# Optimization experiments

Measured on AMD Instinct MI355X. Metric: run time of the kernel, lower is better.

Reference implementation:

```python
import jax, jax.numpy as jnp
import numpy as np

N = 50000
E = 800000
NFEAT = 128
NHID = 64
NCLASS = 40


def setup_inputs() -> dict:
    key = jax.random.key(0)
    ks = jax.random.split(key, 12)
    return {
        "x": jax.random.normal(ks[0], (N, NFEAT), dtype=jnp.float32),
        "M": jax.random.uniform(ks[1], (N, 1), dtype=jnp.float32),
        "AM": jax.random.uniform(ks[2], (N, 1), dtype=jnp.float32),
        "adj_vals": jax.random.uniform(ks[3], (E,), dtype=jnp.float32),
        "adjZ_vals": jax.random.uniform(ks[4], (E,), dtype=jnp.float32),
        "W0": jax.random.normal(ks[5], (NFEAT, NFEAT), dtype=jnp.float32) * (1.414 / np.sqrt(NFEAT)),
        "b0": jnp.zeros((NFEAT,), dtype=jnp.float32),
        "W1": jax.random.normal(ks[6], (NFEAT, NHID), dtype=jnp.float32) * (1.414 / np.sqrt(NFEAT)),
        "b1": jnp.zeros((NHID,), dtype=jnp.float32),
        "W2": jax.random.normal(ks[7], (NHID, NCLASS), dtype=jnp.float32) * (1.0 / np.sqrt(NHID)),
        "b2": jnp.zeros((NCLASS,), dtype=jnp.float32),
        "row": jax.random.randint(ks[8], (E,), 0, N, dtype=jnp.int32),
        "col": jax.random.randint(ks[9], (E,), 0, N, dtype=jnp.int32),
    }


def _spmm(vals, row, col, X, n):
    # sparse (COO) @ dense: out[r] = sum_e vals[e] * X[col[e]] for row[e]==r
    return jax.ops.segment_sum(vals[:, None] * X[col], row, num_segments=n)


def reference(x, M, AM, adj_vals, adjZ_vals, W0, b0, W1, b1, W2, b2, row, col):
    n = x.shape[0]
    # gc0: PaGConv(nfeat->nfeat) on adjZ, then ReLU (dropout is identity in eval)
    h = _spmm(adjZ_vals, row, col, M * x, n) * AM
    h = jax.nn.relu(h @ W0 + b0)
    # gc1: PaGConv(nfeat->nhid) on adjZ, then ReLU
    h = _spmm(adjZ_vals, row, col, M * h, n) * AM
    h = jax.nn.relu(h @ W1 + b1)
    # gc2: plain GConv(nhid->nclass) on adj
    h = _spmm(adj_vals, row, col, h, n)
    h = h @ W2 + b2
    return jax.nn.log_softmax(h, axis=1)
```

## Files before the change

kernel.cpp:

```cpp
#include <hip/hip_runtime.h>
#include <hip/hip_bf16.h>
#include <math.h>


__device__ __forceinline__ float rl_f(float v, int j) {
    return __builtin_bit_cast(float,
        __builtin_amdgcn_readlane(__builtin_bit_cast(int, v), j));
}
__device__ __forceinline__ int rl_i(int v, int j) {
    return __builtin_amdgcn_readlane(v, j);
}
__device__ __forceinline__ unsigned short f2bf(float f) {
    unsigned u = __builtin_bit_cast(unsigned, f);
    u += 0x7fffu + ((u >> 16) & 1u);
    return (unsigned short)(u >> 16);
}
__device__ __forceinline__ float bf_lo(unsigned u) {
    return __builtin_bit_cast(float, u << 16);
}
__device__ __forceinline__ float bf_hi(unsigned u) {
    return __builtin_bit_cast(float, u & 0xffff0000u);
}


template <int K, int COLS, int CPT, bool MSCALE>
__device__ __forceinline__ void gemm_body(float* __restrict__ smem,
                                          const float* __restrict__ A,
                                          const float* __restrict__ Mv,
                                          const float* __restrict__ W,
                                          unsigned short* __restrict__ out, int n, int bid) {
    constexpr int TC = COLS / CPT;
    constexpr int RG = 256 / TC;
    constexpr int RPT = 8;
    constexpr int ROWS = RG * RPT;
    constexpr int KT = 32;
    constexpr int AP = KT + 4;
    static_assert(COLS % CPT == 0 && 256 % TC == 0, "bad tiling");

    float* As = smem;
    float* Ws = smem + ROWS * AP;

    const int t = threadIdx.x;
    const int rg = t / TC;
    const int c0 = (t % TC) * CPT;
    const int r0 = bid * ROWS;

    float acc[RPT][CPT];
#pragma unroll
    for (int i = 0; i < RPT; ++i)
#pragma unroll
        for (int c = 0; c < CPT; ++c) acc[i][c] = 0.0f;

    for (int k0 = 0; k0 < K; k0 += KT) {
        __syncthreads();
        for (int e = t; e < ROWS * (KT / 4); e += 256) {
            const int row = e / (KT / 4);
            const int kq = e % (KT / 4);
            const int r = r0 + row;
            float4 v = make_float4(0.f, 0.f, 0.f, 0.f);
            if (r < n) {
                v = *(const float4*)&A[(size_t)r * K + k0 + kq * 4];
                if constexpr (MSCALE) {
                    const float m = Mv[r];
                    v.x *= m; v.y *= m; v.z *= m; v.w *= m;
                }
            }
            *(float4*)&As[row * AP + kq * 4] = v;
        }
        for (int i = t * 4; i < KT * COLS; i += 1024)
            *(float4*)&Ws[i] = *(const float4*)&W[(size_t)k0 * COLS + i];
        __syncthreads();

#pragma unroll
        for (int kk = 0; kk < KT; kk += 4) {
            float w[4][CPT];
#pragma unroll
            for (int kj = 0; kj < 4; ++kj)
#pragma unroll
                for (int c = 0; c < CPT; ++c)
                    w[kj][c] = Ws[(kk + kj) * COLS + c0 + c];
#pragma unroll
            for (int i = 0; i < RPT; ++i) {
                const float4 av = *(const float4*)&As[(rg + i * RG) * AP + kk];
#pragma unroll
                for (int c = 0; c < CPT; ++c) {
                    acc[i][c] += av.x * w[0][c];
                    acc[i][c] += av.y * w[1][c];
                    acc[i][c] += av.z * w[2][c];
                    acc[i][c] += av.w * w[3][c];
                }
            }
        }
    }

#pragma unroll
    for (int i = 0; i < RPT; ++i) {
        const int r = r0 + rg + i * RG;
        if (r >= n) continue;
        if constexpr (CPT == 4) {
            ushort4 o;
            o.x = f2bf(acc[i][0]); o.y = f2bf(acc[i][1]);
            o.z = f2bf(acc[i][2]); o.w = f2bf(acc[i][3]);
            *(ushort4*)&out[(size_t)r * COLS + c0] = o;
        } else {
#pragma unroll
            for (int c = 0; c < CPT; ++c)
                out[(size_t)r * COLS + c0 + c] = f2bf(acc[i][c]);
        }
    }
}

template <int K, int COLS, int CPT, bool MSCALE>
__launch_bounds__(256)
__global__ void gemm_tile(const float* __restrict__ A, const float* __restrict__ Mv,
                          const float* __restrict__ W, unsigned short* __restrict__ out, int n) {
    constexpr int TC = COLS / CPT;
    constexpr int RG = 256 / TC;
    constexpr int ROWS = RG * 8;
    __shared__ float smem[ROWS * 36 + 32 * COLS];
    gemm_body<K, COLS, CPT, MSCALE>(smem, A, Mv, W, out, n, blockIdx.x);
}


__launch_bounds__(256)
__global__ void gemm0_hist(const float* __restrict__ x, const float* __restrict__ Mv,
                           const float* __restrict__ W0, unsigned short* __restrict__ t_buf,
                           const int* __restrict__ row, int* __restrict__ cnt,
                           int* __restrict__ pos_local, int n, int E, int gemmBlocks) {
    __shared__ float smem[64 * 36 + 32 * 128];
    const int b = blockIdx.x;
    if (b < gemmBlocks) {
        gemm_body<128, 128, 4, true>(smem, x, Mv, W0, t_buf, n, b);
    } else {
        const int e = (b - gemmBlocks) * 256 + threadIdx.x;
        if (e < E) pos_local[e] = atomicAdd(&cnt[row[e]], 1);
    }
}


__global__ void scan_part(const int* __restrict__ cnt, int* __restrict__ out,
                          int* __restrict__ bsums, int n) {
    __shared__ int sdata[256];
    const int t = threadIdx.x;
    const int base = blockIdx.x * 1024 + t * 4;
    int v[4];
#pragma unroll
    for (int i = 0; i < 4; ++i) v[i] = (base + i < n) ? cnt[base + i] : 0;
    int tsum = v[0] + v[1] + v[2] + v[3];
    sdata[t] = tsum;
    __syncthreads();
    for (int off = 1; off < 256; off <<= 1) {
        int x = (t >= off) ? sdata[t - off] : 0;
        __syncthreads();
        sdata[t] += x;
        __syncthreads();
    }
    int run = sdata[t] - tsum;
    if (t == 255) bsums[blockIdx.x] = sdata[t];
#pragma unroll
    for (int i = 0; i < 4; ++i) {
        if (base + i < n) out[base + i] = run;
        run += v[i];
    }
}

__global__ void scan_top(int* __restrict__ bs, int nb) {
    int t = threadIdx.x;
    int orig = (t < nb) ? bs[t] : 0;
    int v = orig;
#pragma unroll
    for (int off = 1; off < 64; off <<= 1) {
        int x = __shfl_up(v, off);
        if (t >= off) v += x;
    }
    if (t < nb) bs[t] = v - orig;
}

__global__ void scan_add(int* __restrict__ rp, const int* __restrict__ bs,
                         int n, int total) {
    int i = blockIdx.x * blockDim.x + threadIdx.x;
    if (i < n) rp[i] += bs[i >> 10];
    if (i == 0) rp[n] = total;
}


__global__ void scatter_kernel(const int* __restrict__ row, const int* __restrict__ col,
                               const float* __restrict__ vA, const float* __restrict__ vZ,
                               const int* __restrict__ rp, const int* __restrict__ pos_local,
                               float* __restrict__ packed, int E) {
    int e = blockIdx.x * blockDim.x + threadIdx.x;
    if (e >= E) return;
    const int pos = rp[row[e]] + pos_local[e];
    float3 pk;
    pk.x = __int_as_float(col[e]);
    pk.y = vZ[e];
    pk.z = vA[e];
    *(float3*)&packed[(size_t)3 * pos] = pk;
}


__launch_bounds__(256)
__global__ void spmm128_kernel(const float* __restrict__ packed,
                               const int* __restrict__ rp, const unsigned short* __restrict__ X,
                               const float* __restrict__ AM, const float* __restrict__ bias,
                               float* __restrict__ out, int n) {
    const int lane = threadIdx.x & 63;
    const int r = (int)((blockIdx.x * (unsigned)blockDim.x + threadIdx.x) >> 6);
    if (r >= n) return;
    const int s = __builtin_amdgcn_readfirstlane(rp[r]);
    const int e = __builtin_amdgcn_readfirstlane(rp[r + 1]);

    float acc0 = 0.0f, acc1 = 0.0f;
    for (int base = s; base < e; base += 64) {
        const int nn = min(64, e - base);
        int ci = 0; float vf = 0.0f;
        if (lane < nn) {
            const float3 pk = *(const float3*)&packed[(size_t)3 * (base + lane)];
            ci = __builtin_bit_cast(int, pk.x);
            vf = pk.y;
        }
        int j = 0;
        for (; j + 8 <= nn; j += 8) {
            unsigned u[8];
#pragma unroll
            for (int q = 0; q < 8; ++q) {
                const int cq = rl_i(ci, j + q);
                u[q] = *(const unsigned*)(X + (size_t)cq * 128 + lane * 2);
            }
#pragma unroll
            for (int q = 0; q < 8; ++q) {
                const float vq = rl_f(vf, j + q);
                acc0 += vq * bf_lo(u[q]);
                acc1 += vq * bf_hi(u[q]);
            }
        }
        for (; j < nn; ++j) {
            const int cq = rl_i(ci, j);
            const float vq = rl_f(vf, j);
            const unsigned u = *(const unsigned*)(X + (size_t)cq * 128 + lane * 2);
            acc0 += vq * bf_lo(u);
            acc1 += vq * bf_hi(u);
        }
    }

    const float am = AM[r];
    float o0 = acc0 * am + bias[2 * lane];
    float o1 = acc1 * am + bias[2 * lane + 1];
    o0 = fmaxf(o0, 0.0f); o1 = fmaxf(o1, 0.0f);
    *(float2*)(out + (size_t)r * 128 + lane * 2) = make_float2(o0, o1);
}


__launch_bounds__(256)
__global__ void spmm64_kernel(const float* __restrict__ packed,
                              const int* __restrict__ rp, const unsigned short* __restrict__ X,
                              const float* __restrict__ AM, const float* __restrict__ bias,
                              float* __restrict__ out, int n) {
    const int lane = threadIdx.x & 63;
    const int g = lane >> 5;
    const int ls = lane & 31;
    const int r = (int)((blockIdx.x * (unsigned)blockDim.x + threadIdx.x) >> 6);
    if (r >= n) return;
    const int s = __builtin_amdgcn_readfirstlane(rp[r]);
    const int e = __builtin_amdgcn_readfirstlane(rp[r + 1]);

    float acc0 = 0.0f, acc1 = 0.0f;
    for (int base = s; base < e; base += 64) {
        const int nn = min(64, e - base);
        int ci = 0; float vf = 0.0f;
        if (lane < nn) {
            const float3 pk = *(const float3*)&packed[(size_t)3 * (base + lane)];
            ci = __builtin_bit_cast(int, pk.x);
            vf = pk.y;
        }
        for (int j = 0; j < nn; j += 8) {
#pragma unroll
            for (int q = 0; q < 4; ++q) {
                const int jj = j + 2 * q + g;
                const bool ok = jj < nn;
                const int idx = jj & 63;
                const int c = __shfl(ci, idx);
                const float v = __shfl(vf, idx);
                if (ok) {
                    const unsigned u = *(const unsigned*)(X + (size_t)c * 64 + ls * 2);
                    acc0 += v * bf_lo(u);
                    acc1 += v * bf_hi(u);
                }
            }
        }
    }
    acc0 += __shfl_xor(acc0, 32);
    acc1 += __shfl_xor(acc1, 32);

    if (lane < 32) {
        const float am = AM[r];
        float o0 = acc0 * am + bias[2 * ls];
        float o1 = acc1 * am + bias[2 * ls + 1];
        o0 = fmaxf(o0, 0.0f); o1 = fmaxf(o1, 0.0f);
        *(float2*)(out + (size_t)r * 64 + ls * 2) = make_float2(o0, o1);
    }
}


__launch_bounds__(256)
__global__ void spmm40_kernel(const float* __restrict__ packed,
                              const int* __restrict__ rp, const unsigned short* __restrict__ X,
                              const float* __restrict__ bias,
                              float* __restrict__ out, int n) {
    const int lane = threadIdx.x & 63;
    const int g = lane / 20;
    const int ls = lane - 20 * g;
    const bool active = g < 3;
    const int r = (int)((blockIdx.x * (unsigned)blockDim.x + threadIdx.x) >> 6);
    if (r >= n) return;
    const int s = __builtin_amdgcn_readfirstlane(rp[r]);
    const int e = __builtin_amdgcn_readfirstlane(rp[r + 1]);

    float acc0 = 0.0f, acc1 = 0.0f;
    for (int base = s; base < e; base += 64) {
        const int nn = min(64, e - base);
        int ci = 0; float vf = 0.0f;
        if (lane < nn) {
            const float3 pk = *(const float3*)&packed[(size_t)3 * (base + lane)];
            ci = __builtin_bit_cast(int, pk.x);
            vf = pk.z;
        }
        for (int j = 0; j < nn; j += 12) {
#pragma unroll
            for (int q = 0; q < 4; ++q) {
                const int jj = j + 3 * q + g;
                const bool ok = active && jj < nn;
                const int idx = jj & 63;
                const int c = __shfl(ci, idx);
                const float v = __shfl(vf, idx);
                if (ok) {
                    const unsigned u = *(const unsigned*)(X + (size_t)c * 40 + ls * 2);
                    acc0 += v * bf_lo(u);
                    acc1 += v * bf_hi(u);
                }
            }
        }
    }
    {
        const float a1 = __shfl(acc0, (lane + 20) & 63);
        const float a2 = __shfl(acc0, (lane + 40) & 63);
        const float b1 = __shfl(acc1, (lane + 20) & 63);
        const float b2 = __shfl(acc1, (lane + 40) & 63);
        acc0 += a1 + a2;
        acc1 += b1 + b2;
    }

    const bool own = lane < 20;
    const float vv0 = own ? (acc0 + bias[2 * ls]) : -INFINITY;
    const float vv1 = own ? (acc1 + bias[2 * ls + 1]) : -INFINITY;
    float mx = fmaxf(vv0, vv1);
#pragma unroll
    for (int off = 32; off > 0; off >>= 1) mx = fmaxf(mx, __shfl_xor(mx, off));
    float sum = own ? (expf(vv0 - mx) + expf(vv1 - mx)) : 0.0f;
#pragma unroll
    for (int off = 32; off > 0; off >>= 1) sum += __shfl_xor(sum, off);
    if (own) {
        const float lse = mx + logf(sum);
        *(float2*)(out + (size_t)r * 40 + ls * 2) = make_float2(vv0 - lse, vv1 - lse);
    }
}


extern "C" void kernel_launch(void* const* d_in, const int* in_sizes, int n_in,
                              void* d_out, int out_size, void* d_ws, size_t ws_size,
                              hipStream_t stream) {
    const float* x    = (const float*)d_in[0];
    const float* M    = (const float*)d_in[1];
    const float* AM   = (const float*)d_in[2];
    const float* adjv = (const float*)d_in[3];
    const float* adjZ = (const float*)d_in[4];
    const float* W0   = (const float*)d_in[5];
    const float* b0   = (const float*)d_in[6];
    const float* W1   = (const float*)d_in[7];
    const float* b1   = (const float*)d_in[8];
    const float* W2   = (const float*)d_in[9];
    const float* b2   = (const float*)d_in[10];
    const int* row    = (const int*)d_in[11];
    const int* col    = (const int*)d_in[12];
    float* out = (float*)d_out;

    const int n = in_sizes[1];
    const int E = in_sizes[3];

    float* t_f   = (float*)d_ws;
    unsigned short* t_buf = (unsigned short*)t_f;
    float* h_buf = t_f + (size_t)n * 128;
    int* cnt     = (int*)(h_buf + (size_t)n * 128);
    int* rp      = cnt + n;
    int* bsums   = rp + (n + 1);
    float* packed = (float*)(bsums + 64);
    int* pos_local = (int*)h_buf;

    hipMemsetAsync(cnt, 0, (size_t)n * sizeof(int), stream);

    const int gemm0Blocks = (n + 63) / 64;
    const int histBlocks  = (E + 255) / 256;
    gemm0_hist<<<gemm0Blocks + histBlocks, 256, 0, stream>>>(x, M, W0, t_buf, row, cnt,
                                                             pos_local, n, E, gemm0Blocks);

    const int nblk = (n + 1023) >> 10;
    scan_part<<<nblk, 256, 0, stream>>>(cnt, rp, bsums, n);
    scan_top<<<1, 64, 0, stream>>>(bsums, nblk);
    scan_add<<<(n + 255) / 256, 256, 0, stream>>>(rp, bsums, n, E);
    scatter_kernel<<<(E + 255) / 256, 256, 0, stream>>>(row, col, adjv, adjZ, rp,
                                                        pos_local, packed, E);

    const int spmmBlocks = (n + 3) / 4;

    spmm128_kernel<<<spmmBlocks, 256, 0, stream>>>(packed, rp, t_buf, AM, b0, h_buf, n);
    gemm_tile<128, 64, 4, true><<<(n + 127) / 128, 256, 0, stream>>>(h_buf, M, W1, t_buf, n);
    spmm64_kernel<<<spmmBlocks, 256, 0, stream>>>(packed, rp, t_buf, AM, b1, h_buf, n);
    gemm_tile<64, 40, 5, false><<<(n + 255) / 256, 256, 0, stream>>>(h_buf, nullptr, W2, t_buf, n);
    spmm40_kernel<<<spmmBlocks, 256, 0, stream>>>(packed, rp, t_buf, b2, out, n);
}
```

Before: 289.8 us.

## Replace FP32 tiled GEMMs with bf16 MFMA GEMMs and bf16 intermediate activations

Replaces the shared-memory FP32 GEMM tiles with MFMA 16x16x32 bf16 matrix instructions, using weights pre-transposed and converted to bf16 by a new small prep kernel. The SpMM kernels now write their ReLU outputs as packed bf16 instead of fp32, and the M row-scaling is folded into spmm128's epilogue, which halves intermediate traffic and lets the GEMMs read bf16 directly. Values are clamped before bf16 conversion. The cost is an extra kernel launch and lower precision in the GEMM inputs.

```diff
diff --git a/kernel.cpp b/kernel.cpp
--- a/kernel.cpp
+++ b/kernel.cpp
@@ -2,6 +2,9 @@
 #include <hip/hip_bf16.h>
 #include <math.h>
 
+
+typedef __attribute__((ext_vector_type(8))) short bf16x8;
+typedef __attribute__((ext_vector_type(4))) float f32x4;
 
 __device__ __forceinline__ float rl_f(float v, int j) {
     return __builtin_bit_cast(float,
@@ -15,122 +18,124 @@
     u += 0x7fffu + ((u >> 16) & 1u);
     return (unsigned short)(u >> 16);
 }
+__device__ __forceinline__ unsigned pack2bf(float lo, float hi) {
+    return (unsigned)f2bf(lo) | ((unsigned)f2bf(hi) << 16);
+}
 __device__ __forceinline__ float bf_lo(unsigned u) {
     return __builtin_bit_cast(float, u << 16);
 }
 __device__ __forceinline__ float bf_hi(unsigned u) {
     return __builtin_bit_cast(float, u & 0xffff0000u);
 }
-
-
-template <int K, int COLS, int CPT, bool MSCALE>
-__device__ __forceinline__ void gemm_body(float* __restrict__ smem,
-                                          const float* __restrict__ A,
-                                          const float* __restrict__ Mv,
-                                          const float* __restrict__ W,
-                                          unsigned short* __restrict__ out, int n, int bid) {
-    constexpr int TC = COLS / CPT;
-    constexpr int RG = 256 / TC;
-    constexpr int RPT = 8;
-    constexpr int ROWS = RG * RPT;
-    constexpr int KT = 32;
-    constexpr int AP = KT + 4;
-    static_assert(COLS % CPT == 0 && 256 % TC == 0, "bad tiling");
-
-    float* As = smem;
-    float* Ws = smem + ROWS * AP;
-
-    const int t = threadIdx.x;
-    const int rg = t / TC;
-    const int c0 = (t % TC) * CPT;
-    const int r0 = bid * ROWS;
-
-    float acc[RPT][CPT];
-#pragma unroll
-    for (int i = 0; i < RPT; ++i)
-#pragma unroll
-        for (int c = 0; c < CPT; ++c) acc[i][c] = 0.0f;
-
-    for (int k0 = 0; k0 < K; k0 += KT) {
-        __syncthreads();
-        for (int e = t; e < ROWS * (KT / 4); e += 256) {
-            const int row = e / (KT / 4);
-            const int kq = e % (KT / 4);
-            const int r = r0 + row;
-            float4 v = make_float4(0.f, 0.f, 0.f, 0.f);
-            if (r < n) {
-                v = *(const float4*)&A[(size_t)r * K + k0 + kq * 4];
-                if constexpr (MSCALE) {
-                    const float m = Mv[r];
-                    v.x *= m; v.y *= m; v.z *= m; v.w *= m;
-                }
+__device__ __forceinline__ float clampf(float v) {
+    return fminf(fmaxf(v, -1e30f), 1e30f);
+}
+
+
+__global__ void prep_wt(const float* __restrict__ W0, const float* __restrict__ W1,
+                        const float* __restrict__ W2,
+                        unsigned short* __restrict__ wt0, unsigned short* __restrict__ wt1,
+                        unsigned short* __restrict__ wt2) {
+    int idx = blockIdx.x * 256 + threadIdx.x;
+    if (idx < 128 * 128) {
+        int nn = idx >> 7, k = idx & 127;
+        wt0[idx] = f2bf(W0[k * 128 + nn]);
+    }
+    idx -= 128 * 128;
+    if (idx >= 0 && idx < 64 * 128) {
+        int nn = idx >> 7, k = idx & 127;
+        wt1[idx] = f2bf(W1[k * 64 + nn]);
+    }
+    idx -= 64 * 128;
+    if (idx >= 0 && idx < 48 * 64) {
+        int nn = idx >> 6, k = idx & 63;
+        wt2[idx] = (nn < 40) ? f2bf(W2[k * 40 + nn]) : (unsigned short)0;
+    }
+}
+
+
+template <int K, int COLS, int NTPAD, bool ABF16, bool MSCALE>
+__device__ __forceinline__ void gemm_mfma_body(const void* __restrict__ Asrc,
+                                               const float* __restrict__ Mv,
+                                               const unsigned short* __restrict__ Wt,
+                                               unsigned short* __restrict__ outp,
+                                               int n, int bid) {
+    constexpr int KS = K / 32;
+    const int lane = threadIdx.x & 63;
+    const int wid = threadIdx.x >> 6;
+    const int m15 = lane & 15;
+    const int q = lane >> 4;
+    const int rA = bid * 64 + wid * 16 + m15;
+
+    bf16x8 a[KS];
+    if constexpr (ABF16) {
+        const unsigned short* A = (const unsigned short*)Asrc;
+#pragma unroll
+        for (int ks = 0; ks < KS; ++ks) {
+            uint4 z = make_uint4(0u, 0u, 0u, 0u);
+            if (rA < n) z = *(const uint4*)(A + (size_t)rA * K + ks * 32 + q * 8);
+            a[ks] = __builtin_bit_cast(bf16x8, z);
+        }
+    } else {
+        const float* A = (const float*)Asrc;
+        float m = 1.0f;
+        if constexpr (MSCALE) { if (rA < n) m = Mv[rA]; }
+#pragma unroll
+        for (int ks = 0; ks < KS; ++ks) {
+            float4 lo = make_float4(0.f, 0.f, 0.f, 0.f);
+            float4 hi = make_float4(0.f, 0.f, 0.f, 0.f);
+            if (rA < n) {
+                lo = *(const float4*)(A + (size_t)rA * K + ks * 32 + q * 8);
+                hi = *(const float4*)(A + (size_t)rA * K + ks * 32 + q * 8 + 4);
             }
-            *(float4*)&As[row * AP + kq * 4] = v;
-        }
-        for (int i = t * 4; i < KT * COLS; i += 1024)
-            *(float4*)&Ws[i] = *(const float4*)&W[(size_t)k0 * COLS + i];
-        __syncthreads();
-
-#pragma unroll
-        for (int kk = 0; kk < KT; kk += 4) {
-            float w[4][CPT];
-#pragma unroll
-            for (int kj = 0; kj < 4; ++kj)
-#pragma unroll
-                for (int c = 0; c < CPT; ++c)
-                    w[kj][c] = Ws[(kk + kj) * COLS + c0 + c];
-#pragma unroll
-            for (int i = 0; i < RPT; ++i) {
-                const float4 av = *(const float4*)&As[(rg + i * RG) * AP + kk];
-#pragma unroll
-                for (int c = 0; c < CPT; ++c) {
-                    acc[i][c] += av.x * w[0][c];
-                    acc[i][c] += av.y * w[1][c];
-                    acc[i][c] += av.z * w[2][c];
-                    acc[i][c] += av.w * w[3][c];
-                }
-            }
-        }
-    }
-
-#pragma unroll
-    for (int i = 0; i < RPT; ++i) {
-        const int r = r0 + rg + i * RG;
-        if (r >= n) continue;
-        if constexpr (CPT == 4) {
-            ushort4 o;
-            o.x = f2bf(acc[i][0]); o.y = f2bf(acc[i][1]);
-            o.z = f2bf(acc[i][2]); o.w = f2bf(acc[i][3]);
-            *(ushort4*)&out[(size_t)r * COLS + c0] = o;
-        } else {
-#pragma unroll
-            for (int c = 0; c < CPT; ++c)
-                out[(size_t)r * COLS + c0 + c] = f2bf(acc[i][c]);
-        }
-    }
-}
-
-template <int K, int COLS, int CPT, bool MSCALE>
+            union { bf16x8 v; unsigned short u[8]; } pk;
+            pk.u[0] = f2bf(lo.x * m); pk.u[1] = f2bf(lo.y * m);
+            pk.u[2] = f2bf(lo.z * m); pk.u[3] = f2bf(lo.w * m);
+            pk.u[4] = f2bf(hi.x * m); pk.u[5] = f2bf(hi.y * m);
+            pk.u[6] = f2bf(hi.z * m); pk.u[7] = f2bf(hi.w * m);
+            a[ks] = pk.v;
+        }
+    }
+
+#pragma unroll
+    for (int nt = 0; nt < NTPAD / 16; ++nt) {
+        f32x4 acc = {0.f, 0.f, 0.f, 0.f};
+        const int bn = nt * 16 + m15;
+#pragma unroll
+        for (int ks = 0; ks < KS; ++ks) {
+            const uint4 z = *(const uint4*)(Wt + (size_t)bn * K + ks * 32 + q * 8);
+            const bf16x8 b = __builtin_bit_cast(bf16x8, z);
+            acc = __builtin_amdgcn_mfma_f32_16x16x32_bf16(a[ks], b, acc, 0, 0, 0);
+        }
+        const int gc = nt * 16 + m15;
+#pragma unroll
+        for (int rr = 0; rr < 4; ++rr) {
+            const int gr = bid * 64 + wid * 16 + q * 4 + rr;
+            bool ok = gr < n;
+            if constexpr (NTPAD != COLS) ok = ok && (gc < COLS);
+            if (ok) outp[(size_t)gr * COLS + gc] = f2bf(clampf(acc[rr]));
+        }
+    }
+}
+
+template <int K, int COLS, int NTPAD, bool ABF16, bool MSCALE>
 __launch_bounds__(256)
-__global__ void gemm_tile(const float* __restrict__ A, const float* __restrict__ Mv,
-                          const float* __restrict__ W, unsigned short* __restrict__ out, int n) {
-    constexpr int TC = COLS / CPT;
-    constexpr int RG = 256 / TC;
-    constexpr int ROWS = RG * 8;
-    __shared__ float smem[ROWS * 36 + 32 * COLS];
-    gemm_body<K, COLS, CPT, MSCALE>(smem, A, Mv, W, out, n, blockIdx.x);
+__global__ void gemm_mfma(const void* __restrict__ A, const float* __restrict__ Mv,
+                          const unsigned short* __restrict__ Wt,
+                          unsigned short* __restrict__ out, int n) {
+    gemm_mfma_body<K, COLS, NTPAD, ABF16, MSCALE>(A, Mv, Wt, out, n, blockIdx.x);
 }
 
 
 __launch_bounds__(256)
 __global__ void gemm0_hist(const float* __restrict__ x, const float* __restrict__ Mv,
-                           const float* __restrict__ W0, unsigned short* __restrict__ t_buf,
+                           const unsigned short* __restrict__ Wt0,
+                           unsigned short* __restrict__ t_buf,
                            const int* __restrict__ row, int* __restrict__ cnt,
                            int* __restrict__ pos_local, int n, int E, int gemmBlocks) {
-    __shared__ float smem[64 * 36 + 32 * 128];
     const int b = blockIdx.x;
     if (b < gemmBlocks) {
-        gemm_body<128, 128, 4, true>(smem, x, Mv, W0, t_buf, n, b);
+        gemm_mfma_body<128, 128, 128, false, true>(x, Mv, Wt0, t_buf, n, b);
     } else {
         const int e = (b - gemmBlocks) * 256 + threadIdx.x;
         if (e < E) pos_local[e] = atomicAdd(&cnt[row[e]], 1);
@@ -202,8 +207,9 @@
 __launch_bounds__(256)
 __global__ void spmm128_kernel(const float* __restrict__ packed,
                                const int* __restrict__ rp, const unsigned short* __restrict__ X,
-                               const float* __restrict__ AM, const float* __restrict__ bias,
-                               float* __restrict__ out, int n) {
+                               const float* __restrict__ AM, const float* __restrict__ Mv,
+                               const float* __restrict__ bias,
+                               unsigned short* __restrict__ out, int n) {
     const int lane = threadIdx.x & 63;
     const int r = (int)((blockIdx.x * (unsigned)blockDim.x + threadIdx.x) >> 6);
     if (r >= n) return;
@@ -244,10 +250,10 @@
     }
 
     const float am = AM[r];
-    float o0 = acc0 * am + bias[2 * lane];
-    float o1 = acc1 * am + bias[2 * lane + 1];
-    o0 = fmaxf(o0, 0.0f); o1 = fmaxf(o1, 0.0f);
-    *(float2*)(out + (size_t)r * 128 + lane * 2) = make_float2(o0, o1);
+    const float mr = Mv[r];
+    const float o0 = fminf(fmaxf((acc0 * am + bias[2 * lane]) * mr, 0.0f), 1e30f);
+    const float o1 = fminf(fmaxf((acc1 * am + bias[2 * lane + 1]) * mr, 0.0f), 1e30f);
+    ((unsigned*)out)[(size_t)r * 64 + lane] = pack2bf(o0, o1);
 }
 
 
@@ -255,7 +261,7 @@
 __global__ void spmm64_kernel(const float* __restrict__ packed,
                               const int* __restrict__ rp, const unsigned short* __restrict__ X,
                               const float* __restrict__ AM, const float* __restrict__ bias,
-                              float* __restrict__ out, int n) {
+                              unsigned short* __restrict__ out, int n) {
     const int lane = threadIdx.x & 63;
     const int g = lane >> 5;
     const int ls = lane & 31;
@@ -294,10 +300,9 @@
 
     if (lane < 32) {
         const float am = AM[r];
-        float o0 = acc0 * am + bias[2 * ls];
-        float o1 = acc1 * am + bias[2 * ls + 1];
-        o0 = fmaxf(o0, 0.0f); o1 = fmaxf(o1, 0.0f);
-        *(float2*)(out + (size_t)r * 64 + ls * 2) = make_float2(o0, o1);
+        const float o0 = fminf(fmaxf(acc0 * am + bias[2 * ls], 0.0f), 1e30f);
+        const float o1 = fminf(fmaxf(acc1 * am + bias[2 * ls + 1], 0.0f), 1e30f);
+        ((unsigned*)out)[(size_t)r * 32 + ls] = pack2bf(o0, o1);
     }
 }
 
@@ -351,8 +356,8 @@
     }
 
     const bool own = lane < 20;
-    const float vv0 = own ? (acc0 + bias[2 * ls]) : -INFINITY;
-    const float vv1 = own ? (acc1 + bias[2 * ls + 1]) : -INFINITY;
+    const float vv0 = own ? fminf(fmaxf(acc0 + bias[2 * ls], -1e30f), 1e30f) : -INFINITY;
+    const float vv1 = own ? fminf(fmaxf(acc1 + bias[2 * ls + 1], -1e30f), 1e30f) : -INFINITY;
     float mx = fmaxf(vv0, vv1);
 #pragma unroll
     for (int off = 32; off > 0; off >>= 1) mx = fmaxf(mx, __shfl_xor(mx, off));
@@ -389,18 +394,24 @@
 
     float* t_f   = (float*)d_ws;
     unsigned short* t_buf = (unsigned short*)t_f;
-    float* h_buf = t_f + (size_t)n * 128;
-    int* cnt     = (int*)(h_buf + (size_t)n * 128);
+    unsigned short* wt0 = t_buf + (size_t)n * 128;
+    unsigned short* wt1 = wt0 + 128 * 128;
+    unsigned short* wt2 = wt1 + 64 * 128;
+    float* h_f   = t_f + (size_t)n * 128;
+    unsigned short* h_buf = (unsigned short*)h_f;
+    int* cnt     = (int*)(h_f + (size_t)n * 128);
     int* rp      = cnt + n;
     int* bsums   = rp + (n + 1);
     float* packed = (float*)(bsums + 64);
-    int* pos_local = (int*)h_buf;
+    int* pos_local = (int*)h_f;
 
     hipMemsetAsync(cnt, 0, (size_t)n * sizeof(int), stream);
+    prep_wt<<<(128 * 128 + 64 * 128 + 48 * 64 + 255) / 256, 256, 0, stream>>>(
+        W0, W1, W2, wt0, wt1, wt2);
 
     const int gemm0Blocks = (n + 63) / 64;
     const int histBlocks  = (E + 255) / 256;
-    gemm0_hist<<<gemm0Blocks + histBlocks, 256, 0, stream>>>(x, M, W0, t_buf, row, cnt,
+    gemm0_hist<<<gemm0Blocks + histBlocks, 256, 0, stream>>>(x, M, wt0, t_buf, row, cnt,
                                                              pos_local, n, E, gemm0Blocks);
 
     const int nblk = (n + 1023) >> 10;
@@ -411,10 +422,13 @@
                                                         pos_local, packed, E);
 
     const int spmmBlocks = (n + 3) / 4;
-
-    spmm128_kernel<<<spmmBlocks, 256, 0, stream>>>(packed, rp, t_buf, AM, b0, h_buf, n);
-    gemm_tile<128, 64, 4, true><<<(n + 127) / 128, 256, 0, stream>>>(h_buf, M, W1, t_buf, n);
+    const int gemmBlocks = (n + 63) / 64;
+
+    spmm128_kernel<<<spmmBlocks, 256, 0, stream>>>(packed, rp, t_buf, AM, M, b0, h_buf, n);
+    gemm_mfma<128, 64, 64, true, false><<<gemmBlocks, 256, 0, stream>>>(h_buf, nullptr, wt1,
+                                                                        t_buf, n);
     spmm64_kernel<<<spmmBlocks, 256, 0, stream>>>(packed, rp, t_buf, AM, b1, h_buf, n);
-    gemm_tile<64, 40, 5, false><<<(n + 255) / 256, 256, 0, stream>>>(h_buf, nullptr, W2, t_buf, n);
+    gemm_mfma<64, 40, 48, true, false><<<gemmBlocks, 256, 0, stream>>>(h_buf, nullptr, wt2,
+                                                                       t_buf, n);
     spmm40_kernel<<<spmmBlocks, 256, 0, stream>>>(packed, rp, t_buf, b2, out, n);
 }
```

New measurement: 284.0 us. 1.02x faster.
